# Optimization experiments

Hardware: AMD Instinct MI355X
Metric: run time of the kernel (lower is better)

## Reference

```python
import jax, jax.numpy as jnp
import numpy as np

B, D, H, W = 32, 96, 96, 96
MAX_POINTS = 512
NUM_CLASSES = 512
# e3nn spherical-harmonic 'integral' normalization constants
C0 = 0.28209479177387814   # 1/(2*sqrt(pi))
C1 = 0.4886025119029199    # sqrt(3/(4*pi))
C2 = 0.6307831305050401    # sqrt(5/(4*pi))
SQ3 = 1.7320508075688772

# (multiplicity, irrep dim) blocks for each irreps layout
BLOCKS_IN = [(16, 1), (8, 3), (4, 5)]   # 16x0e + 8x1o + 4x2e = 60
BLOCKS_H1 = [(32, 1), (8, 3), (4, 5)]   # 76
BLOCKS_H2 = [(64, 1), (4, 3), (2, 5)]   # 86


def setup_inputs() -> dict:
    key = jax.random.key(0)
    ks = jax.random.split(key, 12)
    n = jax.random.normal
    return {
        "x": jax.random.uniform(ks[0], (B, 1, D, H, W), dtype=jnp.float32),
        "W1_0e": n(ks[1], (16, 32)), "W1_1o": n(ks[2], (8, 8)), "W1_2e": n(ks[3], (4, 4)),
        "W2_0e": n(ks[4], (32, 64)), "W2_1o": n(ks[5], (8, 4)), "W2_2e": n(ks[6], (4, 2)),
        "W3_0e": n(ks[7], (64, 128)),
        "fc1_w": n(ks[8], (128, 64)) * 0.05, "fc1_b": jnp.zeros((64,), jnp.float32),
        "fc2_w": n(ks[9], (64, NUM_CLASSES)) * 0.05, "fc2_b": jnp.zeros((NUM_CLASSES,), jnp.float32),
    }


def _topk_pointcloud(x):
    # topk sampling path: highest-density voxels (threshold filter is a no-op
    # for top-k when enough voxels pass, which holds here). x: (B,1,D,H,W)
    vol = x[:, 0]
    flat = vol.reshape(vol.shape[0], -1)
    vals, idx = jax.lax.top_k(flat, MAX_POINTS)          # (B,N)
    z = idx // (H * W)
    rem = idx % (H * W)
    y = rem // W
    xw = rem % W
    coords = jnp.stack([z, y, xw], axis=-1).astype(jnp.float32)  # (B,N,3)
    center = jnp.array([D, H, W], jnp.float32) / 2.0
    scale = float(max(D, H, W)) / 2.0
    points = (coords - center) / scale
    return points, vals


def _point_features(pts, vals):
    # pts: (B,N,3) normalized coords, vals: (B,N) densities -> (B,N,60)
    v = vals[..., None]
    denom = vals.sum(axis=1, keepdims=True)
    com = (pts * v).sum(axis=1) / jnp.maximum(denom, 1e-12)      # (B,3)
    c = pts - com[:, None, :]
    r = jnp.maximum(jnp.linalg.norm(c, axis=-1), 1e-6)           # r_safe (B,N)
    rr = r[..., None]
    d = c / rr                                                   # unit directions
    dx, dy, dz = d[..., 0], d[..., 1], d[..., 2]
    sh1 = C1 * d                                                 # l=1 SH, e3nn order (x,y,z)
    sh2 = C2 * jnp.stack([
        SQ3 * dx * dz,
        SQ3 * dx * dy,
        dy * dy - 0.5 * (dx * dx + dz * dz),
        SQ3 * dy * dz,
        0.5 * SQ3 * (dz * dz - dx * dx),
    ], axis=-1)                                                  # (B,N,5)
    l1pr = jnp.log1p(r)
    sh0 = jnp.full_like(vals, C0)
    scalars = jnp.stack([
        vals, r, sh0, vals * r, vals ** 2, l1pr, jnp.sqrt(vals + 1e-6),
        r ** 2, vals * sh0, jnp.exp(-r), vals ** 3, jnp.sqrt(r),
        vals * l1pr, jax.nn.sigmoid(vals), jax.nn.sigmoid(r), vals * r ** 2,
    ], axis=-1)                                                  # (B,N,16)
    vectors = jnp.concatenate([
        c, c * v, sh1, c * rr, d, d * v, c * v ** 2, sh1 * rr,
    ], axis=-1)                                                  # (B,N,24)
    tensors = jnp.concatenate([
        sh2, sh2 * v, sh2 * rr, sh2 * l1pr[..., None],
    ], axis=-1)                                                  # (B,N,20)
    return jnp.concatenate([scalars, vectors, tensors], axis=-1)


def _irreps_linear(feat, blocks, weights):
    # e3nn o3.Linear: block-diagonal per-irrep linear, one path per block,
    # path normalization 1/sqrt(mul_in). Blocks laid out mul-major.
    outs = []
    start = 0
    for (mul_in, dim), Wb in zip(blocks, weights):
        blk = feat[..., start:start + mul_in * dim]
        blk = blk.reshape(*feat.shape[:-1], mul_in, dim)
        out = jnp.einsum('bnui,uv->bnvi', blk, Wb) / np.sqrt(mul_in).astype(np.float32)
        outs.append(out.reshape(*feat.shape[:-1], -1))
        start += mul_in * dim
    return jnp.concatenate(outs, axis=-1)


def reference(x, W1_0e, W1_1o, W1_2e, W2_0e, W2_1o, W2_2e, W3_0e,
              fc1_w, fc1_b, fc2_w, fc2_b):
    pts, vals = _topk_pointcloud(x)
    feat = _point_features(pts, vals)                    # (B,512,60)
    h = _irreps_linear(feat, BLOCKS_IN, [W1_0e, W1_1o, W1_2e])   # (B,512,76)
    h = _irreps_linear(h, BLOCKS_H1, [W2_0e, W2_1o, W2_2e])      # (B,512,86)
    # layer3 -> 128x0e: only the 0e path exists, 1o/2e inputs are dropped
    h = _irreps_linear(h[..., :64], [(64, 1)], [W3_0e])          # (B,512,128)
    pooled = h.max(axis=1)                               # (B,128)
    hid = jax.nn.relu(pooled @ fc1_w + fc1_b)            # dropout is eval-mode identity
    logits = hid @ fc2_w + fc2_b
    return logits, feat
```

## Files before the change

### kernel.cpp

```cpp
#include <hip/hip_runtime.h>
#include <hip/hip_bf16.h>
#include <stdint.h>

#define NVOX   884736
#define NB     32
#define NPTS   512
#define CAP    4096
#define THRV   0.9990234375f
#define THR_TOP 0x3F7FFFFFu
#define BPB    216
#define SLOT   64
#define LBUF   80
#define NBUCK  128

#define C0c  0.28209479177387814f
#define C1c  0.4886025119029199f
#define C2c  0.6307831305050401f
#define SQ3c 1.7320508075688772f

typedef unsigned long long u64;
typedef unsigned int u32;

__global__ __launch_bounds__(256) void k_collect(const float* __restrict__ x,
                                                 u64* __restrict__ cand,
                                                 u32* __restrict__ counts,
                                                 const float* __restrict__ W1,
                                                 const float* __restrict__ W2,
                                                 const float* __restrict__ W3,
                                                 float* __restrict__ Mg) {
  const int b   = blockIdx.y;
  const int blk = blockIdx.x;
  const int tid = threadIdx.x;
  __shared__ u64 lbuf[LBUF];
  __shared__ float Tm[16 * 64];
  __shared__ int lcnt;
  if (tid == 0) lcnt = 0;
  __syncthreads();

  const float4* xb = reinterpret_cast<const float4*>(x + (size_t)b * NVOX);
  const int t0 = blk * 1024 + tid;
  float4 q[4];
  #pragma unroll
  for (int it = 0; it < 4; ++it) q[it] = xb[t0 + it * 256];

  #pragma unroll
  for (int it = 0; it < 4; ++it) {
    const float4 qq = q[it];
    const u32 base = (u32)(t0 + it * 256) * 4u;
    if (qq.x >= THRV) { int p = atomicAdd(&lcnt, 1); if (p < LBUF) lbuf[p] = ((u64)__float_as_uint(qq.x) << 32) | (u64)(~(base      )); }
    if (qq.y >= THRV) { int p = atomicAdd(&lcnt, 1); if (p < LBUF) lbuf[p] = ((u64)__float_as_uint(qq.y) << 32) | (u64)(~(base + 1u)); }
    if (qq.z >= THRV) { int p = atomicAdd(&lcnt, 1); if (p < LBUF) lbuf[p] = ((u64)__float_as_uint(qq.z) << 32) | (u64)(~(base + 2u)); }
    if (qq.w >= THRV) { int p = atomicAdd(&lcnt, 1); if (p < LBUF) lbuf[p] = ((u64)__float_as_uint(qq.w) << 32) | (u64)(~(base + 3u)); }
  }
  __syncthreads();

  const int slot = b * BPB + blk;
  const int n = lcnt;
  const int wn = (n <= SLOT) ? n : SLOT;
  if (tid < wn) cand[(size_t)slot * SLOT + tid] = lbuf[tid];
  if (tid == 0) counts[slot] = (n <= SLOT) ? (u32)n : (u32)(SLOT + 1);

  if (blk == 0 && b == 0) {
    const float s1c = 1.0f / (4.0f * sqrtf(32.0f));
    for (int e = tid; e < 16 * 64; e += 256) {
      const int u = e >> 6, j = e & 63;
      float s = 0.f;
      for (int k = 0; k < 32; ++k) s += W1[u * 32 + k] * W2[k * 64 + j];
      Tm[e] = s * s1c;
    }
    __syncthreads();
    for (int e = tid; e < 16 * 128; e += 256) {
      const int u = e >> 7, vv = e & 127;
      float s = 0.f;
      for (int j = 0; j < 64; ++j) s += Tm[u * 64 + j] * W3[j * 128 + vv];
      Mg[e] = s * 0.125f;
    }
  }
}

__global__ __launch_bounds__(512) void k_selfeat(const float* __restrict__ x,
                                                 const u64* __restrict__ cand,
                                                 const u32* __restrict__ counts,
                                                 const float* __restrict__ Mg,
                                                 float* __restrict__ ppart,
                                                 float* __restrict__ dout) {
  const int p8  = blockIdx.x;
  const int b   = blockIdx.y;
  const int tid = threadIdx.x;

  __shared__ u64 lk[CAP];
  __shared__ u64 lk2[CAP];
  __shared__ u64 sk[NPTS];
  __shared__ u32 sA[256], sB[256];
  __shared__ u32 scnt[BPB], spref[BPB];
  __shared__ u32 bc[NBUCK], bbx[NBUCK], bp[NBUCK], bA[NBUCK], bB[NBUCK];
  __shared__ float rbuf[8][4];
  __shared__ float comv[4];
  __shared__ float Ms[16 * 128];
  __shared__ __align__(16) float fsb[64][20];
  __shared__ float pr[4][128];
  __shared__ int sbad, sC;
  __shared__ u32 sthr;

  for (int e = tid; e < 16 * 128; e += 512) Ms[e] = Mg[e];

  u32 myc = 0;
  if (tid == 0) sbad = 0;
  if (tid < 256) { myc = (tid < BPB) ? counts[b * BPB + tid] : 0u; sA[tid] = myc; }
  __syncthreads();
  if (tid < BPB && myc > SLOT) atomicOr(&sbad, 1);
  u32 *ssrc = sA, *sdst = sB;
  for (int off = 1; off < 256; off <<= 1) {
    if (tid < 256) sdst[tid] = ssrc[tid] + ((tid >= off) ? ssrc[tid - off] : 0u);
    __syncthreads();
    u32* t = ssrc; ssrc = sdst; sdst = t;
  }
  const int total = (int)ssrc[255];
  if (tid < BPB) { scnt[tid] = myc; spref[tid] = ssrc[tid] - myc; }
  __syncthreads();

  int C;
  if (!sbad && total >= NPTS && total <= CAP) {
    C = total;
    for (int s = tid >> 1; s < BPB; s += 256) {
      const u32 c = scnt[s], p = spref[s];
      const u64* src = cand + (size_t)(b * BPB + s) * SLOT;
      for (u32 k = (u32)(tid & 1); k < c; k += 2) lk[p + k] = src[k];
    }
    __syncthreads();
  } else {
    u32* hist = reinterpret_cast<u32*>(lk);
    for (int i = tid; i < 4096; i += 512) hist[i] = 0u;
    __syncthreads();
    const u32* xb = reinterpret_cast<const u32*>(x) + (size_t)b * NVOX;
    for (int i = tid; i < NVOX; i += 512) {
      const u32 bits = xb[i];
      u32 key;
      if (bits >= 0x3F800000u) key = 0u;
      else { const u32 dd = THR_TOP - bits; key = dd >> 8; if (key > 4095u) key = 4095u; }
      atomicAdd(&hist[key], 1u);
    }
    __syncthreads();
    if (tid == 0) {
      u32 cum = 0; int kt = 4095;
      for (int k = 0; k < 4096; ++k) { cum += hist[k]; if (cum >= (u32)NPTS) { kt = k; break; } }
      sthr = (kt >= 4095) ? 0u : (0x3F800000u - ((u32)(kt + 1) << 8));
      sC = 0;
    }
    __syncthreads();
    const u32 thr = sthr;
    for (int i = tid; i < NVOX; i += 512) {
      const u32 bits = xb[i];
      if (bits >= thr) {
        const int p = atomicAdd(&sC, 1);
        if (p < CAP) lk[p] = ((u64)bits << 32) | (u64)(~(u32)i);
      }
    }
    __syncthreads();
    C = sC < CAP ? sC : CAP;
    __syncthreads();
  }

  if (tid < NBUCK) bc[tid] = 0u;
  __syncthreads();
  for (int i = tid; i < C; i += 512) {
    const u32 bits = (u32)(lk[i] >> 32);
    u32 bk = (THR_TOP - bits) >> 7; if (bk > (NBUCK - 1)) bk = NBUCK - 1;
    atomicAdd(&bc[bk], 1u);
  }
  __syncthreads();
  if (tid < NBUCK) bA[tid] = bc[tid];
  __syncthreads();
  u32 *bsrc = bA, *bdst = bB;
  for (int off = 1; off < NBUCK; off <<= 1) {
    if (tid < NBUCK) bdst[tid] = bsrc[tid] + ((tid >= off) ? bsrc[tid - off] : 0u);
    __syncthreads();
    u32* t = bsrc; bsrc = bdst; bdst = t;
  }
  if (tid < NBUCK) { bbx[tid] = bsrc[tid] - bc[tid]; bp[tid] = bsrc[tid] - bc[tid]; }
  __syncthreads();
  for (int i = tid; i < C; i += 512) {
    const u64 ki = lk[i];
    const u32 bits = (u32)(ki >> 32);
    u32 bk = (THR_TOP - bits) >> 7; if (bk > (NBUCK - 1)) bk = NBUCK - 1;
    const u32 p = atomicAdd(&bp[bk], 1u);
    lk2[p] = ki;
  }
  __syncthreads();
  for (int i = tid; i < C; i += 512) {
    const u64 ki = lk2[i];
    const u32 bits = (u32)(ki >> 32);
    u32 bk = (THR_TOP - bits) >> 7; if (bk > (NBUCK - 1)) bk = NBUCK - 1;
    const u32 lo = bbx[bk], hi = lo + bc[bk];
    int rank = (int)lo;
    for (u32 j = lo; j < hi; ++j) rank += (lk2[j] > ki) ? 1 : 0;
    if (rank < NPTS) sk[rank] = ki;
  }
  __syncthreads();

  {
    const u64 key = sk[tid];
    const u32 bits = (u32)(key >> 32);
    const u32 idx  = ~((u32)key);
    const float v  = __uint_as_float(bits);
    const u32 z = idx / 9216u, rem = idx % 9216u, yy = rem / 96u, xw = rem % 96u;
    const float p0 = ((float)z  - 48.f) / 48.f;
    const float p1 = ((float)yy - 48.f) / 48.f;
    const float p2 = ((float)xw - 48.f) / 48.f;
    float sv = v, s0 = p0 * v, s1 = p1 * v, s2 = p2 * v;
    for (int off = 32; off > 0; off >>= 1) {
      sv += __shfl_down(sv, off);
      s0 += __shfl_down(s0, off);
      s1 += __shfl_down(s1, off);
      s2 += __shfl_down(s2, off);
    }
    const int w = tid >> 6, ln = tid & 63;
    if (ln == 0) { rbuf[w][0] = sv; rbuf[w][1] = s0; rbuf[w][2] = s1; rbuf[w][3] = s2; }
    __syncthreads();
    if (tid == 0) {
      float tv = 0.f, t0s = 0.f, t1s = 0.f, t2s = 0.f;
      for (int wv = 0; wv < 8; ++wv) { tv += rbuf[wv][0]; t0s += rbuf[wv][1]; t1s += rbuf[wv][2]; t2s += rbuf[wv][3]; }
      const float dnm = fmaxf(tv, 1e-12f);
      comv[0] = t0s / dnm; comv[1] = t1s / dnm; comv[2] = t2s / dnm;
    }
    __syncthreads();
  }

  const int pl = tid >> 3, cg = tid & 7;
  const int gp = b * NPTS + p8 * 64 + pl;
  const u64 key = sk[p8 * 64 + pl];
  const u32 bits = (u32)(key >> 32);
  const u32 idx  = ~((u32)key);
  const float v  = __uint_as_float(bits);
  const u32 z = idx / 9216u, rem = idx % 9216u, yy = rem / 96u, xw = rem % 96u;
  const float c0 = ((float)z  - 48.f) / 48.f - comv[0];
  const float c1 = ((float)yy - 48.f) / 48.f - comv[1];
  const float c2 = ((float)xw - 48.f) / 48.f - comv[2];
  const float r = fmaxf(sqrtf(c0 * c0 + c1 * c1 + c2 * c2), 1e-6f);
  const float inv = 1.0f / r;
  const float d0 = c0 * inv, d1 = c1 * inv, d2 = c2 * inv;
  const float v2 = v * v;
  const float rr2 = r * r;
  const float l1 = log1pf(r);
  const float er = expf(-r);
  const float sgv = 1.0f / (1.0f + expf(-v));
  const float sgr = 1.0f / (1.0f + expf(-r));

  float f[60];
  f[0]=v;      f[1]=r;      f[2]=C0c;     f[3]=v*r;
  f[4]=v2;     f[5]=l1;     f[6]=sqrtf(v + 1e-6f); f[7]=rr2;
  f[8]=v*C0c;  f[9]=er;     f[10]=v2*v;   f[11]=sqrtf(r);
  f[12]=v*l1;  f[13]=sgv;   f[14]=sgr;    f[15]=v*rr2;
  f[16]=c0;        f[17]=c1;        f[18]=c2;
  f[19]=c0*v;      f[20]=c1*v;      f[21]=c2*v;
  f[22]=C1c*d0;    f[23]=C1c*d1;    f[24]=C1c*d2;
  f[25]=c0*r;      f[26]=c1*r;      f[27]=c2*r;
  f[28]=d0;        f[29]=d1;        f[30]=d2;
  f[31]=d0*v;      f[32]=d1*v;      f[33]=d2*v;
  f[34]=c0*v2;     f[35]=c1*v2;     f[36]=c2*v2;
  f[37]=C1c*d0*r;  f[38]=C1c*d1*r;  f[39]=C1c*d2*r;
  const float t0 = C2c * (SQ3c * d0 * d2);
  const float t1 = C2c * (SQ3c * d0 * d1);
  const float t2_ = C2c * (d1 * d1 - 0.5f * (d0 * d0 + d2 * d2));
  const float t3 = C2c * (SQ3c * d1 * d2);
  const float t4 = C2c * (0.5f * SQ3c * (d2 * d2 - d0 * d0));
  f[40]=t0;     f[41]=t1;     f[42]=t2_;     f[43]=t3;     f[44]=t4;
  f[45]=t0*v;   f[46]=t1*v;   f[47]=t2_*v;   f[48]=t3*v;   f[49]=t4*v;
  f[50]=t0*r;   f[51]=t1*r;   f[52]=t2_*r;   f[53]=t3*r;   f[54]=t4*r;
  f[55]=t0*l1;  f[56]=t1*l1;  f[57]=t2_*l1;  f[58]=t3*l1;  f[59]=t4*l1;

  float4* ob = reinterpret_cast<float4*>(dout + 16384 + (size_t)gp * 60);
  #pragma unroll
  for (int k = 0; k < 15; ++k)
    if ((k & 7) == cg) ob[k] = make_float4(f[4*k], f[4*k+1], f[4*k+2], f[4*k+3]);

  #pragma unroll
  for (int k = 0; k < 4; ++k)
    if (k == cg) *reinterpret_cast<float4*>(&fsb[pl][k * 4]) =
        make_float4(f[4*k], f[4*k+1], f[4*k+2], f[4*k+3]);
  __syncthreads();

  const int g = tid >> 7, vv = tid & 127;
  float mreg[16];
  #pragma unroll
  for (int u = 0; u < 16; ++u) mreg[u] = Ms[u * 128 + vv];
  float pm = -3.4e38f;
  for (int n = g; n < 64; n += 4) {
    const float4 a0 = *reinterpret_cast<const float4*>(&fsb[n][0]);
    const float4 a1 = *reinterpret_cast<const float4*>(&fsb[n][4]);
    const float4 a2 = *reinterpret_cast<const float4*>(&fsb[n][8]);
    const float4 a3 = *reinterpret_cast<const float4*>(&fsb[n][12]);
    float acc = a0.x*mreg[0] + a0.y*mreg[1] + a0.z*mreg[2] + a0.w*mreg[3]
              + a1.x*mreg[4] + a1.y*mreg[5] + a1.z*mreg[6] + a1.w*mreg[7]
              + a2.x*mreg[8] + a2.y*mreg[9] + a2.z*mreg[10]+ a2.w*mreg[11]
              + a3.x*mreg[12]+ a3.y*mreg[13]+ a3.z*mreg[14]+ a3.w*mreg[15];
    pm = fmaxf(pm, acc);
  }
  pr[g][vv] = pm;
  __syncthreads();
  if (g == 0)
    ppart[((size_t)b * 8 + p8) * 128 + vv] =
        fmaxf(fmaxf(pr[0][vv], pr[1][vv]), fmaxf(pr[2][vv], pr[3][vv]));
}

__global__ __launch_bounds__(512) void k_head(const float* __restrict__ ppart,
                                              const float* __restrict__ fc1w,
                                              const float* __restrict__ fc1b,
                                              const float* __restrict__ fc2w,
                                              const float* __restrict__ fc2b,
                                              float* __restrict__ dout) {
  const int b = blockIdx.x;
  const int t = threadIdx.x;
  __shared__ float pl[128];
  __shared__ float hid[64];
  if (t < 128) {
    float m = -3.4e38f;
    #pragma unroll
    for (int k = 0; k < 8; ++k) m = fmaxf(m, ppart[((size_t)b * 8 + k) * 128 + t]);
    pl[t] = m;
  }
  __syncthreads();
  if (t < 64) {
    float sh = fc1b[t];
    for (int u = 0; u < 128; ++u) sh += pl[u] * fc1w[u * 64 + t];
    hid[t] = fmaxf(sh, 0.f);
  }
  __syncthreads();
  float sl = fc2b[t];
  for (int j = 0; j < 64; ++j) sl += hid[j] * fc2w[j * 512 + t];
  dout[b * 512 + t] = sl;
}

extern "C" void kernel_launch(void* const* d_in, const int* in_sizes, int n_in,
                              void* d_out, int out_size, void* d_ws, size_t ws_size,
                              hipStream_t stream) {
  const float* x    = (const float*)d_in[0];
  const float* W1   = (const float*)d_in[1];
  const float* W2   = (const float*)d_in[4];
  const float* W3   = (const float*)d_in[7];
  const float* fc1w = (const float*)d_in[8];
  const float* fc1b = (const float*)d_in[9];
  const float* fc2w = (const float*)d_in[10];
  const float* fc2b = (const float*)d_in[11];
  float* out = (float*)d_out;

  uint8_t* ws = (uint8_t*)d_ws;
  u32*   counts = (u32*)ws;
  u64*   cand   = (u64*)(ws + 0x10000);
  float* ppart  = (float*)(ws + 0x3A0000);
  float* Mg     = (float*)(ws + 0x3C0000);

  dim3 g1(BPB, NB);
  k_collect<<<g1, 256, 0, stream>>>(x, cand, counts, W1, W2, W3, Mg);
  dim3 g2(8, NB);
  k_selfeat<<<g2, 512, 0, stream>>>(x, cand, counts, Mg, ppart, out);
  k_head<<<NB, 512, 0, stream>>>(ppart, fc1w, fc1b, fc2w, fc2b, out);
}
```

Measured before the change: 41.51 us.

## Compact candidates via global atomic append and simplify bucket prefix scan

Candidate voxels are now appended into one contiguous per-batch buffer through a global atomic counter, replacing fixed per-block slots. This removes the 216-entry prefix scan and scattered gather in the selection kernel. Bucket counting is fused into the candidate load, and the bucket prefix sum becomes a wavefront shuffle scan. The weight-product precompute moves into a new single-block init kernel that also zeroes the counters, which adds an extra launch and global atomics and makes candidate order nondeterministic.

```diff
diff --git a/kernel.cpp b/kernel.cpp
--- a/kernel.cpp
+++ b/kernel.cpp
@@ -9,9 +9,9 @@
 #define THRV   0.9990234375f
 #define THR_TOP 0x3F7FFFFFu
 #define BPB    216
-#define SLOT   64
 #define LBUF   80
 #define NBUCK  128
+#define CNT_STRIDE 32
 
 #define C0c  0.28209479177387814f
 #define C1c  0.4886025119029199f
@@ -21,19 +21,49 @@
 typedef unsigned long long u64;
 typedef unsigned int u32;
 
+__global__ __launch_bounds__(256) void k_init(u32* __restrict__ cnt,
+                                              const float* __restrict__ W1,
+                                              const float* __restrict__ W2,
+                                              const float* __restrict__ W3,
+                                              float* __restrict__ Mg) {
+  const int tid = threadIdx.x;
+  __shared__ float w2[32 * 64];
+  __shared__ float w3[64 * 128];
+  __shared__ float Tm[16 * 64];
+
+  for (int i = tid; i < NB * CNT_STRIDE; i += 256) cnt[i] = 0u;
+
+  for (int i = tid; i < 32 * 64 / 4; i += 256)
+    reinterpret_cast<float4*>(w2)[i] = reinterpret_cast<const float4*>(W2)[i];
+  for (int i = tid; i < 64 * 128 / 4; i += 256)
+    reinterpret_cast<float4*>(w3)[i] = reinterpret_cast<const float4*>(W3)[i];
+  __syncthreads();
+
+  const float s1c = 1.0f / (4.0f * sqrtf(32.0f));
+  for (int e = tid; e < 16 * 64; e += 256) {
+    const int u = e >> 6, j = e & 63;
+    float s = 0.f;
+    for (int k = 0; k < 32; ++k) s += W1[u * 32 + k] * w2[k * 64 + j];
+    Tm[e] = s * s1c;
+  }
+  __syncthreads();
+  for (int e = tid; e < 16 * 128; e += 256) {
+    const int u = e >> 7, vv = e & 127;
+    float s = 0.f;
+    for (int j = 0; j < 64; ++j) s += Tm[u * 64 + j] * w3[j * 128 + vv];
+    Mg[e] = s * 0.125f;
+  }
+}
+
 __global__ __launch_bounds__(256) void k_collect(const float* __restrict__ x,
                                                  u64* __restrict__ cand,
-                                                 u32* __restrict__ counts,
-                                                 const float* __restrict__ W1,
-                                                 const float* __restrict__ W2,
-                                                 const float* __restrict__ W3,
-                                                 float* __restrict__ Mg) {
+                                                 u32* __restrict__ cnt) {
   const int b   = blockIdx.y;
   const int blk = blockIdx.x;
   const int tid = threadIdx.x;
   __shared__ u64 lbuf[LBUF];
-  __shared__ float Tm[16 * 64];
   __shared__ int lcnt;
+  __shared__ u32 gbase;
   if (tid == 0) lcnt = 0;
   __syncthreads();
 
@@ -54,33 +84,27 @@
   }
   __syncthreads();
 
-  const int slot = b * BPB + blk;
-  const int n = lcnt;
-  const int wn = (n <= SLOT) ? n : SLOT;
-  if (tid < wn) cand[(size_t)slot * SLOT + tid] = lbuf[tid];
-  if (tid == 0) counts[slot] = (n <= SLOT) ? (u32)n : (u32)(SLOT + 1);
-
-  if (blk == 0 && b == 0) {
-    const float s1c = 1.0f / (4.0f * sqrtf(32.0f));
-    for (int e = tid; e < 16 * 64; e += 256) {
-      const int u = e >> 6, j = e & 63;
-      float s = 0.f;
-      for (int k = 0; k < 32; ++k) s += W1[u * 32 + k] * W2[k * 64 + j];
-      Tm[e] = s * s1c;
-    }
-    __syncthreads();
-    for (int e = tid; e < 16 * 128; e += 256) {
-      const int u = e >> 7, vv = e & 127;
-      float s = 0.f;
-      for (int j = 0; j < 64; ++j) s += Tm[u * 64 + j] * W3[j * 128 + vv];
-      Mg[e] = s * 0.125f;
-    }
+  if (tid == 0) {
+    int n = lcnt;
+    if (n > LBUF) {
+      gbase = atomicAdd(&cnt[b * CNT_STRIDE], (u32)LBUF);
+      atomicAdd(&cnt[b * CNT_STRIDE], (u32)(CAP + 1));
+    } else {
+      gbase = n ? atomicAdd(&cnt[b * CNT_STRIDE], (u32)n) : 0u;
+    }
+  }
+  __syncthreads();
+
+  const int n = lcnt < LBUF ? lcnt : LBUF;
+  if (tid < n) {
+    const u32 p = gbase + (u32)tid;
+    if (p < CAP) cand[(size_t)b * CAP + p] = lbuf[tid];
   }
 }
 
 __global__ __launch_bounds__(512) void k_selfeat(const float* __restrict__ x,
                                                  const u64* __restrict__ cand,
-                                                 const u32* __restrict__ counts,
+                                                 const u32* __restrict__ cnt,
                                                  const float* __restrict__ Mg,
                                                  float* __restrict__ ppart,
                                                  float* __restrict__ dout) {
@@ -91,41 +115,27 @@
   __shared__ u64 lk[CAP];
   __shared__ u64 lk2[CAP];
   __shared__ u64 sk[NPTS];
-  __shared__ u32 sA[256], sB[256];
-  __shared__ u32 scnt[BPB], spref[BPB];
-  __shared__ u32 bc[NBUCK], bbx[NBUCK], bp[NBUCK], bA[NBUCK], bB[NBUCK];
+  __shared__ u32 bc[NBUCK], bbx[NBUCK], bp[NBUCK];
   __shared__ float rbuf[8][4];
   __shared__ float comv[4];
   __shared__ float Ms[16 * 128];
   __shared__ __align__(16) float fsb[64][20];
   __shared__ float pr[4][128];
-  __shared__ int sbad, sC;
+  __shared__ int sC;
   __shared__ u32 sthr;
 
   for (int e = tid; e < 16 * 128; e += 512) Ms[e] = Mg[e];
-
-  u32 myc = 0;
-  if (tid == 0) sbad = 0;
-  if (tid < 256) { myc = (tid < BPB) ? counts[b * BPB + tid] : 0u; sA[tid] = myc; }
-  __syncthreads();
-  if (tid < BPB && myc > SLOT) atomicOr(&sbad, 1);
-  u32 *ssrc = sA, *sdst = sB;
-  for (int off = 1; off < 256; off <<= 1) {
-    if (tid < 256) sdst[tid] = ssrc[tid] + ((tid >= off) ? ssrc[tid - off] : 0u);
-    __syncthreads();
-    u32* t = ssrc; ssrc = sdst; sdst = t;
-  }
-  const int total = (int)ssrc[255];
-  if (tid < BPB) { scnt[tid] = myc; spref[tid] = ssrc[tid] - myc; }
-  __syncthreads();
-
-  int C;
-  if (!sbad && total >= NPTS && total <= CAP) {
-    C = total;
-    for (int s = tid >> 1; s < BPB; s += 256) {
-      const u32 c = scnt[s], p = spref[s];
-      const u64* src = cand + (size_t)(b * BPB + s) * SLOT;
-      for (u32 k = (u32)(tid & 1); k < c; k += 2) lk[p + k] = src[k];
+  if (tid < NBUCK) bc[tid] = 0u;
+  __syncthreads();
+
+  int C = (int)cnt[b * CNT_STRIDE];
+
+  if (C >= NPTS && C <= CAP) {
+    for (int i = tid; i < C; i += 512) {
+      const u64 k = cand[(size_t)b * CAP + i];
+      lk[i] = k;
+      u32 bk = (THR_TOP - (u32)(k >> 32)) >> 7; if (bk > (NBUCK - 1)) bk = NBUCK - 1;
+      atomicAdd(&bc[bk], 1u);
     }
     __syncthreads();
   } else {
@@ -158,39 +168,39 @@
     }
     __syncthreads();
     C = sC < CAP ? sC : CAP;
-    __syncthreads();
-  }
-
-  if (tid < NBUCK) bc[tid] = 0u;
-  __syncthreads();
-  for (int i = tid; i < C; i += 512) {
-    const u32 bits = (u32)(lk[i] >> 32);
-    u32 bk = (THR_TOP - bits) >> 7; if (bk > (NBUCK - 1)) bk = NBUCK - 1;
-    atomicAdd(&bc[bk], 1u);
-  }
-  __syncthreads();
-  if (tid < NBUCK) bA[tid] = bc[tid];
-  __syncthreads();
-  u32 *bsrc = bA, *bdst = bB;
-  for (int off = 1; off < NBUCK; off <<= 1) {
-    if (tid < NBUCK) bdst[tid] = bsrc[tid] + ((tid >= off) ? bsrc[tid - off] : 0u);
-    __syncthreads();
-    u32* t = bsrc; bsrc = bdst; bdst = t;
-  }
-  if (tid < NBUCK) { bbx[tid] = bsrc[tid] - bc[tid]; bp[tid] = bsrc[tid] - bc[tid]; }
-  __syncthreads();
+    for (int i = tid; i < C; i += 512) {
+      u32 bk = (THR_TOP - (u32)(lk[i] >> 32)) >> 7; if (bk > (NBUCK - 1)) bk = NBUCK - 1;
+      atomicAdd(&bc[bk], 1u);
+    }
+    __syncthreads();
+  }
+
+  if (tid < 64) {
+    const u32 b0 = bc[2 * tid], b1 = bc[2 * tid + 1];
+    const u32 s = b0 + b1;
+    u32 incl = s;
+    #pragma unroll
+    for (int off = 1; off < 64; off <<= 1) {
+      const u32 t = __shfl_up(incl, off, 64);
+      if (tid >= off) incl += t;
+    }
+    const u32 excl = incl - s;
+    bbx[2 * tid] = excl;       bbx[2 * tid + 1] = excl + b0;
+    bp[2 * tid]  = excl;       bp[2 * tid + 1]  = excl + b0;
+  }
+  __syncthreads();
+
   for (int i = tid; i < C; i += 512) {
     const u64 ki = lk[i];
-    const u32 bits = (u32)(ki >> 32);
-    u32 bk = (THR_TOP - bits) >> 7; if (bk > (NBUCK - 1)) bk = NBUCK - 1;
+    u32 bk = (THR_TOP - (u32)(ki >> 32)) >> 7; if (bk > (NBUCK - 1)) bk = NBUCK - 1;
     const u32 p = atomicAdd(&bp[bk], 1u);
     lk2[p] = ki;
   }
   __syncthreads();
+
   for (int i = tid; i < C; i += 512) {
     const u64 ki = lk2[i];
-    const u32 bits = (u32)(ki >> 32);
-    u32 bk = (THR_TOP - bits) >> 7; if (bk > (NBUCK - 1)) bk = NBUCK - 1;
+    u32 bk = (THR_TOP - (u32)(ki >> 32)) >> 7; if (bk > (NBUCK - 1)) bk = NBUCK - 1;
     const u32 lo = bbx[bk], hi = lo + bc[bk];
     int rank = (int)lo;
     for (u32 j = lo; j < hi; ++j) rank += (lk2[j] > ki) ? 1 : 0;
@@ -345,14 +355,15 @@
   float* out = (float*)d_out;
 
   uint8_t* ws = (uint8_t*)d_ws;
-  u32*   counts = (u32*)ws;
-  u64*   cand   = (u64*)(ws + 0x10000);
-  float* ppart  = (float*)(ws + 0x3A0000);
-  float* Mg     = (float*)(ws + 0x3C0000);
-
+  u32*   cnt   = (u32*)ws;
+  float* Mg    = (float*)(ws + 0x1000);
+  float* ppart = (float*)(ws + 0x4000);
+  u64*   cand  = (u64*)(ws + 0x100000);
+
+  k_init<<<1, 256, 0, stream>>>(cnt, W1, W2, W3, Mg);
   dim3 g1(BPB, NB);
-  k_collect<<<g1, 256, 0, stream>>>(x, cand, counts, W1, W2, W3, Mg);
+  k_collect<<<g1, 256, 0, stream>>>(x, cand, cnt);
   dim3 g2(8, NB);
-  k_selfeat<<<g2, 512, 0, stream>>>(x, cand, counts, Mg, ppart, out);
+  k_selfeat<<<g2, 512, 0, stream>>>(x, cand, cnt, Mg, ppart, out);
   k_head<<<NB, 512, 0, stream>>>(ppart, fc1w, fc1b, fc2w, fc2b, out);
 }
```

Result: slower. 49.24 us (+18.6%).
